# Kernel optimization log

Hardware: AMD Instinct MI355X
Metric: run time of the kernel (lower is better)

The kernel has to match this reference:

```python
import jax, jax.numpy as jnp
import numpy as np

HIDDEN = 2048
NUM_HEADS = 16
HEAD_DIM = HIDDEN // NUM_HEADS  # 128
ROPE_BASE = 10000.0


def setup_inputs() -> dict:
    key = jax.random.key(0)
    ks = jax.random.split(key, 5)
    B, T, C = 2, 2048, HIDDEN
    scale = 1.0 / np.sqrt(C)
    x = jax.random.normal(ks[0], (B, T, C), dtype=jnp.float32)
    Wq = jax.random.normal(ks[1], (C, C), dtype=jnp.float32) * scale
    Wk = jax.random.normal(ks[2], (C, C), dtype=jnp.float32) * scale
    Wv = jax.random.normal(ks[3], (C, C), dtype=jnp.float32) * scale
    Wo = jax.random.normal(ks[4], (C, C), dtype=jnp.float32) * scale
    return {"x": x, "Wq": Wq, "Wk": Wk, "Wv": Wv, "Wo": Wo}


def _rope_cos_sin(T, dtype):
    # inv_freq: [D/2]; emb: [T, D] = cat(freqs, freqs)
    inv_freq = 1.0 / (ROPE_BASE ** (jnp.arange(0, HEAD_DIM, 2, dtype=jnp.float32) / HEAD_DIM))
    t = jnp.arange(T, dtype=jnp.float32)
    freqs = t[:, None] * inv_freq[None, :]          # [T, D/2]
    emb = jnp.concatenate([freqs, freqs], axis=-1)  # [T, D]
    # broadcast shape [1, T, 1, D] to match q/k [B, T, H, D]
    return jnp.cos(emb)[None, :, None, :].astype(dtype), jnp.sin(emb)[None, :, None, :].astype(dtype)


def _rotate_half(u):
    u1, u2 = jnp.split(u, 2, axis=-1)
    return jnp.concatenate([-u2, u1], axis=-1)


def reference(x, Wq, Wk, Wv, Wo):
    B, T, C = x.shape
    H, D = NUM_HEADS, HEAD_DIM
    # QKV projections (torch Linear: x @ W.T). Weights here stored as [C, C] so use x @ W.
    q = (x @ Wq).reshape(B, T, H, D)
    k = (x @ Wk).reshape(B, T, H, D)
    v = (x @ Wv).reshape(B, T, H, D)
    cos, sin = _rope_cos_sin(T, x.dtype)
    q = q * cos + _rotate_half(q) * sin
    k = k * cos + _rotate_half(k) * sin
    # causal SDPA: scores [B, H, T, T]
    scale = 1.0 / jnp.sqrt(jnp.asarray(D, dtype=x.dtype))
    scores = jnp.einsum('bqhd,bkhd->bhqk', q, k) * scale
    causal = jnp.tril(jnp.ones((T, T), dtype=bool))
    scores = jnp.where(causal[None, None, :, :], scores, jnp.asarray(-jnp.inf, dtype=scores.dtype))
    attn = jax.nn.softmax(scores, axis=-1)
    out = jnp.einsum('bhqk,bkhd->bqhd', attn, v).reshape(B, T, C)
    return out @ Wo
```

## Files before the change

### kernel.cpp

```cpp
#include <hip/hip_runtime.h>
#include <hip/hip_bf16.h>

#define C_DIM 2048
#define NHEAD 16
#define HD 128
#define BB 2
#define TT 2048
#define MM (BB * TT)
#define NQT 32
#define N3 (3 * C_DIM)

typedef short short4v __attribute__((ext_vector_type(4)));
typedef short short8v __attribute__((ext_vector_type(8)));
typedef __bf16 bf16x4 __attribute__((ext_vector_type(4)));
typedef __bf16 bf16x8 __attribute__((ext_vector_type(8)));
typedef float f32x4 __attribute__((ext_vector_type(4)));

#define AS1 __attribute__((address_space(1)))
#define AS3 __attribute__((address_space(3)))

#define VMCNT(n) asm volatile("s_waitcnt vmcnt(" #n ")" ::: "memory")

__device__ __forceinline__ void load_lds16(const void* g, void* l) {
  __builtin_amdgcn_global_load_lds((const AS1 void*)g, (AS3 void*)l, 16, 0, 0);
}

__device__ __forceinline__ short f2bf(float f) {
  union { float f; unsigned u; } v; v.f = f;
  unsigned u = v.u;
  u += 0x7FFFu + ((u >> 16) & 1u);
  return (short)(u >> 16);
}
__device__ __forceinline__ float bf2f(short s) {
  union { unsigned u; float f; } v;
  v.u = ((unsigned)(unsigned short)s) << 16;
  return v.f;
}

__device__ __forceinline__ float exp2_fast(float x) {
  float r;
  asm("v_exp_f32 %0, %1" : "=v"(r) : "v"(x));
  return r;
}

__global__ __launch_bounds__(256) void cvt_x(const float* __restrict__ in,
                                             short* __restrict__ out, int n4) {
  int i = blockIdx.x * 256 + threadIdx.x;
  int stride = gridDim.x * 256;
  for (int idx = i; idx < n4; idx += stride) {
    float4 f = ((const float4*)in)[idx];
    short4v o;
    o[0] = f2bf(f.x); o[1] = f2bf(f.y); o[2] = f2bf(f.z); o[3] = f2bf(f.w);
    ((short4v*)out)[idx] = o;
  }
}

__global__ __launch_bounds__(256) void cvt_w_t(const float* __restrict__ W,
                                               short* __restrict__ Wt) {
  __shared__ float tile[32][33];
  int bx = blockIdx.x;
  int by = blockIdx.y;
  int lx = threadIdx.x & 31;
  int ly = threadIdx.x >> 5;
#pragma unroll
  for (int j = 0; j < 4; ++j) {
    int r = by * 32 + ly + j * 8;
    tile[ly + j * 8][lx] = W[(size_t)r * C_DIM + bx * 32 + lx];
  }
  __syncthreads();
#pragma unroll
  for (int j = 0; j < 4; ++j) {
    int n = bx * 32 + ly + j * 8;
    Wt[(size_t)n * C_DIM + by * 32 + lx] = f2bf(tile[lx][ly + j * 8]);
  }
}

__global__ __launch_bounds__(256) void rope_tab(float2* __restrict__ tab) {
  int idx = blockIdx.x * 256 + threadIdx.x;
  int t = idx >> 6, d = idx & 63;
  float inv = expf(-9.210340371976184f * (float)d * (1.0f / 64.0f));
  float a = (float)t * inv;
  tab[idx] = make_float2(cosf(a), sinf(a));
}

template <bool F32OUT>
__global__ __launch_bounds__(256, 2) void gemm8p(const short* __restrict__ A,
                                                 const short* __restrict__ Bt,
                                                 void* __restrict__ Cout,
                                                 int M, int N, int K, int NBN) {
  __shared__ short sA[2][128 * 64];
  __shared__ short sB[2][128 * 64];
  const int tid = threadIdx.x;
  const int lane = tid & 63;
  const int w = tid >> 6;
  const int wm = w >> 1, wn = w & 1;
  const int r = lane & 15, g = lane >> 4;

  const int wg = blockIdx.x;
  const int mb = wg / NBN, nb = wg % NBN;
  const int m0 = mb * 128, n0 = nb * 128;

  f32x4 acc[4][4] = {};

  auto stage = [&](int buf, int kt) {
#pragma unroll
    for (int j = 0; j < 4; ++j) {
      int p = j * 256 + tid;
      int row = p >> 3;
      int c16 = (p & 7) ^ (row & 7);
      load_lds16(A + (size_t)(m0 + row) * K + kt * 64 + c16 * 8,
                 &sA[buf][(j * 256 + w * 64) * 8]);
    }
#pragma unroll
    for (int j = 0; j < 4; ++j) {
      int p = j * 256 + tid;
      int row = p >> 3;
      int c16 = (p & 7) ^ (row & 7);
      load_lds16(Bt + (size_t)(n0 + row) * K + kt * 64 + c16 * 8,
                 &sB[buf][(j * 256 + w * 64) * 8]);
    }
  };

  auto compute = [&](int buf) {
#pragma unroll
    for (int kk = 0; kk < 2; ++kk) {
      bf16x8 af[4], bv[4];
#pragma unroll
      for (int m = 0; m < 4; ++m) {
        int row = wm * 64 + m * 16 + r;
        af[m] = *(const bf16x8*)((const char*)&sA[buf][0] + row * 128 +
                                 (((kk * 4 + g) ^ (row & 7)) << 4));
      }
#pragma unroll
      for (int n = 0; n < 4; ++n) {
        int row = wn * 64 + n * 16 + r;
        bv[n] = *(const bf16x8*)((const char*)&sB[buf][0] + row * 128 +
                                 (((kk * 4 + g) ^ (row & 7)) << 4));
      }
      __builtin_amdgcn_s_setprio(1);
#pragma unroll
      for (int m = 0; m < 4; ++m)
#pragma unroll
        for (int n = 0; n < 4; ++n)
          acc[m][n] = __builtin_amdgcn_mfma_f32_16x16x32_bf16(af[m], bv[n], acc[m][n], 0, 0, 0);
      __builtin_amdgcn_s_setprio(0);
    }
  };

  const int NT = K >> 6;
  stage(0, 0);
  stage(1, 1);
  VMCNT(8);
  __builtin_amdgcn_s_barrier();

  for (int t = 0; t < NT; ++t) {
    const int cur = t & 1;
    compute(cur);
    if (t + 1 < NT) {
      asm volatile("" ::: "memory");
      __builtin_amdgcn_s_barrier();
      if (t + 2 < NT) {
        stage(cur, t + 2);
        VMCNT(8);
      } else {
        VMCNT(0);
      }
      asm volatile("" ::: "memory");
      __builtin_amdgcn_s_barrier();
    }
  }

#pragma unroll
  for (int m = 0; m < 4; ++m)
#pragma unroll
    for (int n = 0; n < 4; ++n)
#pragma unroll
      for (int q = 0; q < 4; ++q) {
        int row = m0 + wm * 64 + m * 16 + g * 4 + q;
        int col = n0 + wn * 64 + n * 16 + r;
        size_t off = (size_t)row * N + col;
        if constexpr (F32OUT) ((float*)Cout)[off] = acc[m][n][q];
        else ((short*)Cout)[off] = f2bf(acc[m][n][q]);
      }
}

__global__ __launch_bounds__(256) void rope_qk(const short* __restrict__ qkv,
                                               const float2* __restrict__ tab,
                                               short* __restrict__ Qr,
                                               short* __restrict__ Kr) {
  const short* src = qkv + (blockIdx.y ? C_DIM : 0);
  short* dst = blockIdx.y ? Kr : Qr;
  const float qs = blockIdx.y ? 1.0f : 0.12751744f;
  int rid = blockIdx.x * 4 + (threadIdx.x >> 6);
  int lane = threadIdx.x & 63;
  int t = rid & (TT - 1);
  int bh = rid >> 11;
  int b = bh >> 4, h = bh & 15;
  const short* in = src + ((size_t)(b * TT + t)) * N3 + h * HD;
  float f0 = bf2f(in[lane]);
  float f1 = bf2f(in[lane + 64]);
  float2 cs = tab[t * 64 + lane];
  dst[(size_t)rid * HD + lane]      = f2bf((f0 * cs.x - f1 * cs.y) * qs);
  dst[(size_t)rid * HD + lane + 64] = f2bf((f1 * cs.x + f0 * cs.y) * qs);
}

__global__ __launch_bounds__(256) void v_tr(const short* __restrict__ qkv,
                                            short* __restrict__ Vt) {
  __shared__ short tl[64][132];
  int bh = blockIdx.y, b = bh >> 4, h = bh & 15;
  int t0 = blockIdx.x * 64;
  int tid = threadIdx.x;
  const short* vsrc = qkv + 2 * C_DIM;
#pragma unroll
  for (int i = 0; i < 4; ++i) {
    int c = i * 256 + tid;
    int row = c >> 4, cc = c & 15;
    short8v v = *(const short8v*)(vsrc + ((size_t)(b * TT + t0 + row)) * N3 + h * HD + cc * 8);
#pragma unroll
    for (int j = 0; j < 8; ++j) tl[row][cc * 8 + j] = v[j];
  }
  __syncthreads();
  int d = tid >> 1, half = tid & 1;
#pragma unroll
  for (int u = 0; u < 4; ++u) {
    short8v ov;
#pragma unroll
    for (int j = 0; j < 8; ++j) ov[j] = tl[half * 32 + u * 8 + j][d];
    *(short8v*)(Vt + ((size_t)bh * HD + d) * TT + t0 + half * 32 + u * 8) = ov;
  }
}

__global__ __launch_bounds__(256, 3) void attn_one(const short* __restrict__ Qr,
                                                   const short* __restrict__ Kr,
                                                   const short* __restrict__ Vt,
                                                   short* __restrict__ AO) {
  const int bx = blockIdx.x;
  const int j = bx >> 5, bh = bx & 31;
  const int qt = (j & 1) ? (j >> 1) : (NQT - 1 - (j >> 1));
  const int b = bh >> 4, h = bh & 15;
  const int tid = threadIdx.x;
  const int lane = tid & 63;
  const int w = tid >> 6;
  const int r = lane & 15, g = lane >> 4;

  __shared__ short sK[64 * 128];
  __shared__ short sV[128 * 64];
  __shared__ short sP[4][16 * 64];

  bf16x8 qf[4];
  {
    const short* qbp = Qr + ((size_t)bh * TT + qt * 64 + w * 16 + r) * HD + g * 8;
#pragma unroll
    for (int s = 0; s < 4; ++s) qf[s] = *(const bf16x8*)(qbp + s * 32);
  }

  f32x4 o[8] = {};
  float m = -1e30f, l = 0.f;

  short8v kreg[4], vreg[4];
  auto stage_load = [&](int kt) {
#pragma unroll
    for (int i = 0; i < 4; ++i) {
      int c = i * 256 + tid;
      kreg[i] = *(const short8v*)(Kr + ((size_t)bh * TT + kt * 64 + (c >> 4)) * HD + (c & 15) * 8);
    }
#pragma unroll
    for (int i = 0; i < 4; ++i) {
      int c = i * 256 + tid;
      vreg[i] = *(const short8v*)(Vt + ((size_t)bh * HD + (c >> 3)) * TT + kt * 64 + (c & 7) * 8);
    }
  };
  auto stage_write = [&]() {
#pragma unroll
    for (int i = 0; i < 4; ++i) {
      int c = i * 256 + tid;
      int row = c >> 4, cc = c & 15;
      int addr = (row * 256 + cc * 16) ^ ((row & 7) << 4);
      *(short8v*)((char*)sK + addr) = kreg[i];
    }
#pragma unroll
    for (int i = 0; i < 4; ++i) {
      int c = i * 256 + tid;
      int row = c >> 3, cc = c & 7;
      int addr = (row * 128 + cc * 16) ^ ((row & 7) << 4);
      *(short8v*)((char*)sV + addr) = vreg[i];
    }
  };

  char* pw = (char*)&sP[w][0];

  stage_load(0);
  stage_write();
  __syncthreads();

  for (int kt = 0; kt <= qt; ++kt) {
    if (kt < qt) stage_load(kt + 1);

    f32x4 sacc[4] = {};
    __builtin_amdgcn_s_setprio(1);
#pragma unroll
    for (int nf = 0; nf < 4; ++nf) {
#pragma unroll
      for (int ss = 0; ss < 4; ++ss) {
        int krow = nf * 16 + r;
        int addr = (krow * 256 + (ss * 32 + g * 8) * 2) ^ ((krow & 7) << 4);
        bf16x8 kf = *(const bf16x8*)((char*)sK + addr);
        sacc[nf] = __builtin_amdgcn_mfma_f32_16x16x32_bf16(kf, qf[ss], sacc[nf], 0, 0, 0);
      }
    }
    __builtin_amdgcn_s_setprio(0);

    if (kt == qt) {
#pragma unroll
      for (int nf = 0; nf < 4; ++nf)
#pragma unroll
        for (int q = 0; q < 4; ++q)
          if (nf * 16 + g * 4 + q > w * 16 + r) sacc[nf][q] = -1e30f;
    }

    float p01 = fmaxf(fmaxf(sacc[0][0], sacc[0][1]), fmaxf(sacc[0][2], sacc[0][3]));
    float p23 = fmaxf(fmaxf(sacc[1][0], sacc[1][1]), fmaxf(sacc[1][2], sacc[1][3]));
    float p45 = fmaxf(fmaxf(sacc[2][0], sacc[2][1]), fmaxf(sacc[2][2], sacc[2][3]));
    float p67 = fmaxf(fmaxf(sacc[3][0], sacc[3][1]), fmaxf(sacc[3][2], sacc[3][3]));
    float pmax = fmaxf(fmaxf(p01, p23), fmaxf(p45, p67));
    pmax = fmaxf(pmax, __shfl_xor(pmax, 16, 64));
    pmax = fmaxf(pmax, __shfl_xor(pmax, 32, 64));

    if (!__all(pmax - m <= 8.0f)) {
      float mnew = fmaxf(m, pmax);
      float alpha = exp2_fast(m - mnew);
      m = mnew;
      l *= alpha;
#pragma unroll
      for (int q = 0; q < 4; ++q) {
        float aq = __shfl(alpha, (g * 4 + q) | (lane & 48), 64);
#pragma unroll
        for (int nf2 = 0; nf2 < 8; ++nf2) o[nf2][q] *= aq;
      }
    }

    float s16 = 0.f;
#pragma unroll
    for (int nf = 0; nf < 4; ++nf) {
      f32x4 pe;
#pragma unroll
      for (int q = 0; q < 4; ++q) pe[q] = exp2_fast(sacc[nf][q] - m);
      s16 += (pe[0] + pe[1]) + (pe[2] + pe[3]);
      int addr = (r * 128 + nf * 32 + g * 8) ^ ((r & 7) << 4);
      *(bf16x4*)(pw + addr) = __builtin_convertvector(pe, bf16x4);
    }
    float rs = s16;
    rs += __shfl_xor(rs, 16, 64);
    rs += __shfl_xor(rs, 32, 64);
    l += rs;

    __builtin_amdgcn_s_setprio(1);
#pragma unroll
    for (int s2 = 0; s2 < 2; ++s2) {
      int paddr = (r * 128 + s2 * 64 + g * 16) ^ ((r & 7) << 4);
      bf16x8 pa = *(const bf16x8*)(pw + paddr);
#pragma unroll
      for (int nf2 = 0; nf2 < 8; ++nf2) {
        int drow = nf2 * 16 + r;
        int addr = (drow * 128 + (s2 * 32 + g * 8) * 2) ^ ((drow & 7) << 4);
        bf16x8 vb = *(const bf16x8*)((char*)sV + addr);
        o[nf2] = __builtin_amdgcn_mfma_f32_16x16x32_bf16(pa, vb, o[nf2], 0, 0, 0);
      }
    }
    __builtin_amdgcn_s_setprio(0);

    __syncthreads();
    if (kt < qt) {
      stage_write();
      __syncthreads();
    }
  }

  float linv = 1.0f / l;
  float lrow[4];
#pragma unroll
  for (int q = 0; q < 4; ++q)
    lrow[q] = __shfl(linv, (g * 4 + q) | (lane & 48), 64);
#pragma unroll
  for (int nf2 = 0; nf2 < 8; ++nf2)
#pragma unroll
    for (int q = 0; q < 4; ++q) {
      int t = qt * 64 + w * 16 + g * 4 + q;
      int cc = h * HD + nf2 * 16 + r;
      AO[((size_t)b * TT + t) * C_DIM + cc] = f2bf(o[nf2][q] * lrow[q]);
    }
}

extern "C" void kernel_launch(void* const* d_in, const int* in_sizes, int n_in,
                              void* d_out, int out_size, void* d_ws, size_t ws_size,
                              hipStream_t stream) {
  const float* x  = (const float*)d_in[0];
  const float* Wq = (const float*)d_in[1];
  const float* Wk = (const float*)d_in[2];
  const float* Wv = (const float*)d_in[3];
  const float* Wo = (const float*)d_in[4];

  char* ws = (char*)d_ws;
  size_t off = 0;
  auto take = [&](size_t bytes) {
    char* p = ws + off;
    off += (bytes + 255) & ~(size_t)255;
    return p;
  };
  const size_t xe = (size_t)MM * C_DIM;
  const size_t we = (size_t)C_DIM * C_DIM;
  short* xb   = (short*)take(xe * 2);
  short* wqkv = (short*)take(3 * we * 2);
  short* wot  = (short*)take(we * 2);
  short* qkv  = (short*)take(3 * xe * 2);
  short* Qr   = (short*)take(xe * 2);
  short* Kr   = (short*)take(xe * 2);
  short* Vtr  = (short*)take(xe * 2);
  float2* tab = (float2*)take((size_t)TT * 64 * sizeof(float2));
  short* AO   = qkv;

  cvt_x<<<2048, 256, 0, stream>>>(x, xb, (int)(xe / 4));
  cvt_w_t<<<dim3(64, 64), 256, 0, stream>>>(Wq, wqkv);
  cvt_w_t<<<dim3(64, 64), 256, 0, stream>>>(Wk, wqkv + we);
  cvt_w_t<<<dim3(64, 64), 256, 0, stream>>>(Wv, wqkv + 2 * we);
  cvt_w_t<<<dim3(64, 64), 256, 0, stream>>>(Wo, wot);
  rope_tab<<<(TT * 64) / 256, 256, 0, stream>>>(tab);

  gemm8p<false><<<1536, 256, 0, stream>>>(xb, wqkv, qkv, MM, N3, C_DIM, N3 / 128);

  rope_qk<<<dim3(16384, 2), 256, 0, stream>>>(qkv, tab, Qr, Kr);
  v_tr<<<dim3(32, 32), 256, 0, stream>>>(qkv, Vtr);

  attn_one<<<1024, 256, 0, stream>>>(Qr, Kr, Vtr, AO);

  gemm8p<true><<<512, 256, 0, stream>>>(AO, wot, d_out, MM, C_DIM, C_DIM, C_DIM / 128);
}
```

Measured before the change: 293.7 us.

## Coalesce attention output via LDS, vectorize RoPE, fuse weight conversions, move prefetch

The attention kernel now stages its normalized output tile in shared memory and writes it to global memory with 16-byte coalesced stores instead of scattered 2-byte stores. The RoPE kernel loads and stores pairs of bf16 values and gets the rotate-half partner with a cross-lane shuffle, so it issues fewer, wider memory operations. The four weight transpose/convert launches are merged into one 3D-grid launch, and the next K/V tile prefetch is moved to after the QK^T MFMA block. Together these aim to cut memory transaction overhead and launch overhead, with a small risk that the moved prefetch exposes more load latency.

```diff
diff --git a/kernel.cpp b/kernel.cpp
--- a/kernel.cpp
+++ b/kernel.cpp
@@ -55,9 +55,15 @@
   }
 }
 
-__global__ __launch_bounds__(256) void cvt_w_t(const float* __restrict__ W,
-                                               short* __restrict__ Wt) {
+__global__ __launch_bounds__(256) void cvt_w_all(const float* __restrict__ Wq,
+                                                 const float* __restrict__ Wk,
+                                                 const float* __restrict__ Wv,
+                                                 const float* __restrict__ Wo,
+                                                 short* __restrict__ Wt) {
   __shared__ float tile[32][33];
+  int z = blockIdx.z;
+  const float* W = z == 0 ? Wq : z == 1 ? Wk : z == 2 ? Wv : Wo;
+  short* dst = Wt + (size_t)z * C_DIM * C_DIM;
   int bx = blockIdx.x;
   int by = blockIdx.y;
   int lx = threadIdx.x & 31;
@@ -71,7 +77,7 @@
 #pragma unroll
   for (int j = 0; j < 4; ++j) {
     int n = bx * 32 + ly + j * 8;
-    Wt[(size_t)n * C_DIM + by * 32 + lx] = f2bf(tile[lx][ly + j * 8]);
+    dst[(size_t)n * C_DIM + by * 32 + lx] = f2bf(tile[lx][ly + j * 8]);
   }
 }
 
@@ -197,11 +203,18 @@
   int bh = rid >> 11;
   int b = bh >> 4, h = bh & 15;
   const short* in = src + ((size_t)(b * TT + t)) * N3 + h * HD;
-  float f0 = bf2f(in[lane]);
-  float f1 = bf2f(in[lane + 64]);
-  float2 cs = tab[t * 64 + lane];
-  dst[(size_t)rid * HD + lane]      = f2bf((f0 * cs.x - f1 * cs.y) * qs);
-  dst[(size_t)rid * HD + lane + 64] = f2bf((f1 * cs.x + f0 * cs.y) * qs);
+
+  int v = *(const int*)(in + 2 * lane);
+  int pv = __shfl_xor(v, 32, 64);
+  float f0 = bf2f((short)(v & 0xFFFF)),  f1 = bf2f((short)(v >> 16));
+  float p0 = bf2f((short)(pv & 0xFFFF)), p1 = bf2f((short)(pv >> 16));
+  float4 cst = *(const float4*)(tab + (size_t)t * 64 + ((2 * lane) & 63));
+  float s = (lane < 32) ? -1.0f : 1.0f;
+  float o0 = (f0 * cst.x + s * p0 * cst.y) * qs;
+  float o1 = (f1 * cst.z + s * p1 * cst.w) * qs;
+  unsigned out2 = ((unsigned)(unsigned short)f2bf(o0)) |
+                  (((unsigned)(unsigned short)f2bf(o1)) << 16);
+  *(unsigned*)(dst + (size_t)rid * HD + 2 * lane) = out2;
 }
 
 __global__ __launch_bounds__(256) void v_tr(const short* __restrict__ qkv,
@@ -294,8 +307,6 @@
   __syncthreads();
 
   for (int kt = 0; kt <= qt; ++kt) {
-    if (kt < qt) stage_load(kt + 1);
-
     f32x4 sacc[4] = {};
     __builtin_amdgcn_s_setprio(1);
 #pragma unroll
@@ -309,6 +320,8 @@
       }
     }
     __builtin_amdgcn_s_setprio(0);
+
+    if (kt < qt) stage_load(kt + 1);
 
     if (kt == qt) {
 #pragma unroll
@@ -381,14 +394,23 @@
 #pragma unroll
   for (int q = 0; q < 4; ++q)
     lrow[q] = __shfl(linv, (g * 4 + q) | (lane & 48), 64);
+  short* ow = sK + w * 16 * 128;
 #pragma unroll
   for (int nf2 = 0; nf2 < 8; ++nf2)
 #pragma unroll
-    for (int q = 0; q < 4; ++q) {
-      int t = qt * 64 + w * 16 + g * 4 + q;
-      int cc = h * HD + nf2 * 16 + r;
-      AO[((size_t)b * TT + t) * C_DIM + cc] = f2bf(o[nf2][q] * lrow[q]);
-    }
+    for (int q = 0; q < 4; ++q)
+      ow[(g * 4 + q) * 128 + nf2 * 16 + r] = f2bf(o[nf2][q] * lrow[q]);
+  __syncthreads();
+
+#pragma unroll
+  for (int ch = 0; ch < 4; ++ch) {
+    int c = ch * 256 + tid;
+    int orow = c >> 4;
+    int ocol = (c & 15) * 8;
+    int t = qt * 64 + orow;
+    *(short8v*)(AO + ((size_t)b * TT + t) * C_DIM + h * HD + ocol) =
+        *(const short8v*)(sK + orow * 128 + ocol);
+  }
 }
 
 extern "C" void kernel_launch(void* const* d_in, const int* in_sizes, int n_in,
@@ -410,8 +432,8 @@
   const size_t xe = (size_t)MM * C_DIM;
   const size_t we = (size_t)C_DIM * C_DIM;
   short* xb   = (short*)take(xe * 2);
-  short* wqkv = (short*)take(3 * we * 2);
-  short* wot  = (short*)take(we * 2);
+  short* wqkv = (short*)take(4 * we * 2);
+  short* wot  = wqkv + 3 * we;
   short* qkv  = (short*)take(3 * xe * 2);
   short* Qr   = (short*)take(xe * 2);
   short* Kr   = (short*)take(xe * 2);
@@ -420,10 +442,7 @@
   short* AO   = qkv;
 
   cvt_x<<<2048, 256, 0, stream>>>(x, xb, (int)(xe / 4));
-  cvt_w_t<<<dim3(64, 64), 256, 0, stream>>>(Wq, wqkv);
-  cvt_w_t<<<dim3(64, 64), 256, 0, stream>>>(Wk, wqkv + we);
-  cvt_w_t<<<dim3(64, 64), 256, 0, stream>>>(Wv, wqkv + 2 * we);
-  cvt_w_t<<<dim3(64, 64), 256, 0, stream>>>(Wo, wot);
+  cvt_w_all<<<dim3(64, 64, 4), 256, 0, stream>>>(Wq, Wk, Wv, Wo, wqkv);
   rope_tab<<<(TT * 64) / 256, 256, 0, stream>>>(tab);
 
   gemm8p<false><<<1536, 256, 0, stream>>>(xb, wqkv, qkv, MM, N3, C_DIM, N3 / 128);
```

New measurement: 290.1 us. Within noise of the previous version (-1.2%).
